# Kernel optimization log

Hardware: AMD Instinct MI355X
Metric: run time of the kernel (lower is better)

Reference implementation:

```python
import jax, jax.numpy as jnp
import numpy as np

N = 300_000
DEG = 16
E = N * DEG
EPS_W = 1e-12  # guard for zero-distance neighbors
EPS_A = 1e-8   # diagonal regularization of the 3x3 normal matrix


def setup_inputs() -> dict:
    key = jax.random.key(0)
    k1, k2, k3 = jax.random.split(key, 3)
    coordinates = jax.random.normal(k1, (N, 3), dtype=jnp.float32)
    u = jax.random.normal(k2, (N, 1), dtype=jnp.float32)
    # uniform-degree CSR: offsets[i] = i*DEG
    offsets = (jnp.arange(N + 1) * DEG).astype(jnp.int32)
    indices = jax.random.randint(k3, (E,), 0, N, dtype=jnp.int32)
    return {"coordinates": coordinates, "u": u, "offsets": offsets, "indices": indices}


def _mesh_lsq_gradient(coords, values, offsets, indices):
    """Weighted least-squares gradient reconstruction over a CSR neighbor list.

    coords: [N,3], values: [N,C], offsets: [N+1], indices: [E].
    Returns [N,3,C]: per-node gradient of each channel.
    """
    n = coords.shape[0]
    e = indices.shape[0]
    # node id owning each edge: offsets[i] <= e < offsets[i+1]
    seg = jnp.searchsorted(offsets, jnp.arange(e, dtype=offsets.dtype), side='right') - 1
    dx = coords[indices] - coords[seg]            # [E,3]
    dv = values[indices] - values[seg]            # [E,C]
    w = 1.0 / jnp.maximum(jnp.sum(dx * dx, axis=-1), EPS_W)  # inverse-distance^2 weights [E]
    # normal equations: A g = b per node
    A = jax.ops.segment_sum(w[:, None, None] * dx[:, :, None] * dx[:, None, :], seg, num_segments=n)  # [N,3,3]
    b = jax.ops.segment_sum(w[:, None, None] * dx[:, :, None] * dv[:, None, :], seg, num_segments=n)  # [N,3,C]
    A = A + EPS_A * jnp.eye(3, dtype=coords.dtype)
    return jnp.linalg.solve(A, b)  # [N,3,C]


def reference(coordinates, u, offsets, indices):
    coords = jax.lax.stop_gradient(coordinates)  # original does coords.detach()
    vals = u[:, 0:1]                              # squeeze(-1), keep as 1 channel
    first = _mesh_lsq_gradient(coords, vals, offsets, indices)[..., 0]   # [N,3] = (u_x,u_y,u_z)
    # second pass: gradients of all three first derivatives at once (channels)
    second = _mesh_lsq_gradient(coords, first, offsets, indices)         # [N,3,3]; second[:,b,a] = d(du/dx_a)/dx_b
    u_xx = second[:, 0, 0]
    u_yy = second[:, 1, 1]
    u_zz = second[:, 2, 2]
    u_xy = second[:, 1, 0]  # mixed = second_grads[a][:, b] for a<b
    u_xz = second[:, 2, 0]
    u_yz = second[:, 2, 1]
    # columns: [xx, yy, zz, xy, xz, yz] (mixed derivs returned once; module duplicates symmetric keys)
    return jnp.stack([u_xx, u_yy, u_zz, u_xy, u_xz, u_yz], axis=-1)
```

## Files before the change

### kernel.cpp

```cpp
#include <hip/hip_runtime.h>
#include <hip/hip_fp16.h>


constexpr int N_NODES = 300000;
constexpr int DEG = 16;
constexpr float EPS_W = 1e-12f;
constexpr double EPS_A = 1e-8;

typedef float f32x4 __attribute__((ext_vector_type(4)));
typedef float f32x2 __attribute__((ext_vector_type(2)));

__device__ __forceinline__ float redux16(float v) {
    v += __shfl_xor(v, 1, 16);
    v += __shfl_xor(v, 2, 16);
    v += __shfl_xor(v, 4, 16);
    v += __shfl_xor(v, 8, 16);
    return v;
}

__global__ __launch_bounds__(256) void pack_p1(
    const float* __restrict__ coords,
    const float* __restrict__ u,
    float4* __restrict__ p1)
{
    int i = blockIdx.x * 256 + threadIdx.x;
    if (i >= N_NODES) return;
    p1[i] = make_float4(coords[3 * i + 0], coords[3 * i + 1],
                        coords[3 * i + 2], u[i]);
}


__global__ __launch_bounds__(256) void lsq_pass1_x(
    const float4* __restrict__ p1,
    const int*    __restrict__ indices,
    float4*       __restrict__ G,
    f32x4*        __restrict__ M,
    f32x2*        __restrict__ WDX)
{
    int tid  = blockIdx.x * 256 + threadIdx.x;
    int node = tid >> 4;
    int lane = tid & 15;
    if (node >= N_NODES) return;

    float4 c = p1[node];
    int e = node * DEG + lane;
    int j = __builtin_nontemporal_load(indices + e);
    float4 p = p1[j];

    float dx = p.x - c.x, dy = p.y - c.y, dz = p.z - c.z, dv = p.w - c.w;
    float w = 1.0f / fmaxf(dx * dx + dy * dy + dz * dz, EPS_W);
    float wx = w * dx, wy = w * dy, wz = w * dz;

    union { __half h[4]; f32x2 f2; } pk;
    pk.h[0] = __float2half_rn(wx);
    pk.h[1] = __float2half_rn(wy);
    pk.h[2] = __float2half_rn(wz);
    pk.h[3] = __float2half_rn(0.0f);
    __builtin_nontemporal_store(pk.f2, WDX + e);

    float a00 = redux16(wx * dx);
    float a01 = redux16(wx * dy);
    float a02 = redux16(wx * dz);
    float a11 = redux16(wy * dy);
    float a12 = redux16(wy * dz);
    float a22 = redux16(wz * dz);
    float b0  = redux16(wx * dv);
    float b1  = redux16(wy * dv);
    float b2  = redux16(wz * dv);

    if (lane == 0) {
        double A00 = (double)a00 + EPS_A;
        double A11 = (double)a11 + EPS_A;
        double A22 = (double)a22 + EPS_A;
        double A01 = (double)a01, A02 = (double)a02, A12 = (double)a12;
        double j00 = A11 * A22 - A12 * A12;
        double j01 = A02 * A12 - A01 * A22;
        double j02 = A01 * A12 - A02 * A11;
        double j11 = A00 * A22 - A02 * A02;
        double j12 = A01 * A02 - A00 * A12;
        double j22 = A00 * A11 - A01 * A01;
        double det = A00 * j00 + A01 * j01 + A02 * j02;
        double inv = 1.0 / det;
        float m00 = (float)(j00 * inv), m01 = (float)(j01 * inv);
        float m02 = (float)(j02 * inv), m11 = (float)(j11 * inv);
        float m12 = (float)(j12 * inv), m22 = (float)(j22 * inv);
        float g0 = m00 * b0 + m01 * b1 + m02 * b2;
        float g1 = m01 * b0 + m11 * b1 + m12 * b2;
        float g2 = m02 * b0 + m12 * b1 + m22 * b2;
        G[node] = make_float4(g0, g1, g2, 0.0f);
        f32x4 mv0 = {m00, m01, m02, m11};
        f32x4 mv1 = {m12, m22, 0.0f, 0.0f};
        __builtin_nontemporal_store(mv0, M + 2 * node);
        __builtin_nontemporal_store(mv1, M + 2 * node + 1);
    }
}

__global__ __launch_bounds__(256) void lsq_pass2_x(
    const float4* __restrict__ G,
    const f32x4*  __restrict__ M,
    const f32x2*  __restrict__ WDX,
    const int*    __restrict__ indices,
    float*        __restrict__ out)
{
    int tid  = blockIdx.x * 256 + threadIdx.x;
    int node = tid >> 4;
    int lane = tid & 15;
    if (node >= N_NODES) return;

    float4 gi = G[node];
    int e = node * DEG + lane;
    int j = __builtin_nontemporal_load(indices + e);
    union { __half h[4]; f32x2 f2; } pk;
    pk.f2 = __builtin_nontemporal_load(WDX + e);
    float wx = __half2float(pk.h[0]);
    float wy = __half2float(pk.h[1]);
    float wz = __half2float(pk.h[2]);

    float4 gj = G[j];
    float dv0 = gj.x - gi.x, dv1 = gj.y - gi.y, dv2 = gj.z - gi.z;

    float b00 = redux16(wx * dv0);
    float b10 = redux16(wy * dv0);
    float b20 = redux16(wz * dv0);
    float b01 = redux16(wx * dv1);
    float b11 = redux16(wy * dv1);
    float b21 = redux16(wz * dv1);
    float b02 = redux16(wx * dv2);
    float b12 = redux16(wy * dv2);
    float b22 = redux16(wz * dv2);

    if (lane == 0) {
        f32x4 m0 = __builtin_nontemporal_load(M + 2 * node);
        f32x4 m1 = __builtin_nontemporal_load(M + 2 * node + 1);
        float m00 = m0.x, m01 = m0.y, m02 = m0.z, m11 = m0.w;
        float m12 = m1.x, m22 = m1.y;
        float x00 = m00 * b00 + m01 * b10 + m02 * b20;
        float x10 = m01 * b00 + m11 * b10 + m12 * b20;
        float x20 = m02 * b00 + m12 * b10 + m22 * b20;
        float x11 = m01 * b01 + m11 * b11 + m12 * b21;
        float x21 = m02 * b01 + m12 * b11 + m22 * b21;
        float x22 = m02 * b02 + m12 * b12 + m22 * b22;
        f32x2* o2 = (f32x2*)(out + 6 * node);
        f32x2 o0 = {x00, x11};
        f32x2 o1 = {x22, x10};
        f32x2 o2v = {x20, x21};
        __builtin_nontemporal_store(o0, o2 + 0);
        __builtin_nontemporal_store(o1, o2 + 1);
        __builtin_nontemporal_store(o2v, o2 + 2);
    }
}


__global__ __launch_bounds__(256) void lsq_pass1_fb(
    const float4* __restrict__ p1,
    const int*    __restrict__ indices,
    float4*       __restrict__ p2)
{
    int tid  = blockIdx.x * 256 + threadIdx.x;
    int node = tid >> 4;
    int lane = tid & 15;
    if (node >= N_NODES) return;

    float4 c = p1[node];
    int j = __builtin_nontemporal_load(indices + node * DEG + lane);
    float4 p = p1[j];
    float dx = p.x - c.x, dy = p.y - c.y, dz = p.z - c.z, dv = p.w - c.w;
    float w = 1.0f / fmaxf(dx * dx + dy * dy + dz * dz, EPS_W);

    float a00 = redux16(w * dx * dx);
    float a01 = redux16(w * dx * dy);
    float a02 = redux16(w * dx * dz);
    float a11 = redux16(w * dy * dy);
    float a12 = redux16(w * dy * dz);
    float a22 = redux16(w * dz * dz);
    float b0  = redux16(w * dx * dv);
    float b1  = redux16(w * dy * dv);
    float b2  = redux16(w * dz * dv);

    if (lane == 0) {
        double A00 = (double)a00 + EPS_A;
        double A11 = (double)a11 + EPS_A;
        double A22 = (double)a22 + EPS_A;
        double A01 = (double)a01, A02 = (double)a02, A12 = (double)a12;
        double j00 = A11 * A22 - A12 * A12;
        double j01 = A02 * A12 - A01 * A22;
        double j02 = A01 * A12 - A02 * A11;
        double j11 = A00 * A22 - A02 * A02;
        double j12 = A01 * A02 - A00 * A12;
        double j22 = A00 * A11 - A01 * A01;
        double det = A00 * j00 + A01 * j01 + A02 * j02;
        double inv = 1.0 / det;
        float g0 = (float)((j00 * b0 + j01 * b1 + j02 * b2) * inv);
        float g1 = (float)((j01 * b0 + j11 * b1 + j12 * b2) * inv);
        float g2 = (float)((j02 * b0 + j12 * b1 + j22 * b2) * inv);
        p2[2 * node + 0] = make_float4(c.x, c.y, c.z, g0);
        p2[2 * node + 1] = make_float4(g1, g2, 0.0f, 0.0f);
    }
}

__global__ __launch_bounds__(256) void lsq_pass2_fb(
    const float4* __restrict__ p2,
    const int*    __restrict__ indices,
    float*        __restrict__ out)
{
    int tid  = blockIdx.x * 256 + threadIdx.x;
    int node = tid >> 4;
    int lane = tid & 15;
    if (node >= N_NODES) return;

    float4 c0 = p2[2 * node + 0];
    float4 c1 = p2[2 * node + 1];
    int j = __builtin_nontemporal_load(indices + node * DEG + lane);
    float4 r0 = p2[2 * j + 0];
    float4 r1 = p2[2 * j + 1];

    float dx = r0.x - c0.x, dy = r0.y - c0.y, dz = r0.z - c0.z;
    float dv0 = r0.w - c0.w, dv1 = r1.x - c1.x, dv2 = r1.y - c1.y;
    float w = 1.0f / fmaxf(dx * dx + dy * dy + dz * dz, EPS_W);

    float a00 = redux16(w * dx * dx);
    float a01 = redux16(w * dx * dy);
    float a02 = redux16(w * dx * dz);
    float a11 = redux16(w * dy * dy);
    float a12 = redux16(w * dy * dz);
    float a22 = redux16(w * dz * dz);
    float b00 = redux16(w * dx * dv0);
    float b10 = redux16(w * dy * dv0);
    float b20 = redux16(w * dz * dv0);
    float b01 = redux16(w * dx * dv1);
    float b11 = redux16(w * dy * dv1);
    float b21 = redux16(w * dz * dv1);
    float b02 = redux16(w * dx * dv2);
    float b12 = redux16(w * dy * dv2);
    float b22 = redux16(w * dz * dv2);

    if (lane == 0) {
        double A00 = (double)a00 + EPS_A;
        double A11 = (double)a11 + EPS_A;
        double A22 = (double)a22 + EPS_A;
        double A01 = (double)a01, A02 = (double)a02, A12 = (double)a12;
        double j00 = A11 * A22 - A12 * A12;
        double j01 = A02 * A12 - A01 * A22;
        double j02 = A01 * A12 - A02 * A11;
        double j11 = A00 * A22 - A02 * A02;
        double j12 = A01 * A02 - A00 * A12;
        double j22 = A00 * A11 - A01 * A01;
        double det = A00 * j00 + A01 * j01 + A02 * j02;
        double inv = 1.0 / det;
        double x00 = (j00 * b00 + j01 * b10 + j02 * b20) * inv;
        double x10 = (j01 * b00 + j11 * b10 + j12 * b20) * inv;
        double x20 = (j02 * b00 + j12 * b10 + j22 * b20) * inv;
        double x11 = (j01 * b01 + j11 * b11 + j12 * b21) * inv;
        double x21 = (j02 * b01 + j12 * b11 + j22 * b21) * inv;
        double x22 = (j02 * b02 + j12 * b12 + j22 * b22) * inv;
        __builtin_nontemporal_store((float)x00, out + 6 * node + 0);
        __builtin_nontemporal_store((float)x11, out + 6 * node + 1);
        __builtin_nontemporal_store((float)x22, out + 6 * node + 2);
        __builtin_nontemporal_store((float)x10, out + 6 * node + 3);
        __builtin_nontemporal_store((float)x20, out + 6 * node + 4);
        __builtin_nontemporal_store((float)x21, out + 6 * node + 5);
    }
}

extern "C" void kernel_launch(void* const* d_in, const int* in_sizes, int n_in,
                              void* d_out, int out_size, void* d_ws, size_t ws_size,
                              hipStream_t stream) {
    const float* coords  = (const float*)d_in[0];
    const float* u       = (const float*)d_in[1];
    const int*   indices = (const int*)d_in[3];
    float*       out     = (float*)d_out;

    const int block = 256;
    const int grid_edges = (N_NODES * DEG) / block;
    const int grid_nodes = (N_NODES + block - 1) / block;

    const size_t szP1  = (size_t)N_NODES * 16;
    const size_t szG   = (size_t)N_NODES * 16;
    const size_t szM   = (size_t)N_NODES * 32;
    const size_t szWDX = (size_t)N_NODES * DEG * 8;
    const size_t need_main = szP1 + szG + szM + szWDX;

    char* ws = (char*)d_ws;
    float4* p1 = (float4*)ws;
    pack_p1<<<grid_nodes, block, 0, stream>>>(coords, u, p1);

    if (ws_size >= need_main) {
        float4* G   = (float4*)(ws + szP1);
        f32x4*  M   = (f32x4*)(ws + szP1 + szG);
        f32x2*  WDX = (f32x2*)(ws + szP1 + szG + szM);
        lsq_pass1_x<<<grid_edges, block, 0, stream>>>(p1, indices, G, M, WDX);
        lsq_pass2_x<<<grid_edges, block, 0, stream>>>(G, M, WDX, indices, out);
    } else {
        float4* p2 = (float4*)(ws + szP1);
        lsq_pass1_fb<<<grid_edges, block, 0, stream>>>(p1, indices, p2);
        lsq_pass2_fb<<<grid_edges, block, 0, stream>>>(p2, indices, out);
    }
}
```

Measured before the change: 160.8 us.

## Fuse pack and both LSQ passes into one cooperative persistent kernel

Replaces the three-kernel sequence with one cooperative kernel of 1024 blocks that packs inputs, runs pass one, grid-syncs, then runs pass two. Each 16-lane group keeps neighbor indices and fp16-packed weighted dx/dy (plus fp32 wz) in registers, and keeps the inverse normal matrix in shared memory, so the per-edge WDX and M buffers and the second index read are no longer written to or fetched from global memory. This trades kernel-launch boundaries for grid-wide barriers, lower occupancy from a fixed grid with register arrays, and reduced precision on two of the weight components. It falls back to the old path if the cooperative launch fails.

```diff
diff --git a/kernel.cpp b/kernel.cpp
--- a/kernel.cpp
+++ b/kernel.cpp
@@ -1,11 +1,20 @@
 #include <hip/hip_runtime.h>
 #include <hip/hip_fp16.h>
+#include <hip/hip_cooperative_groups.h>
+
+namespace cg = cooperative_groups;
 
 
 constexpr int N_NODES = 300000;
 constexpr int DEG = 16;
 constexpr float EPS_W = 1e-12f;
 constexpr double EPS_A = 1e-8;
+
+constexpr int NBLK = 1024;
+constexpr int TPB  = 256;
+constexpr int GRP  = TPB / 16;
+constexpr int NPB  = (N_NODES + NBLK - 1) / NBLK;
+constexpr int ITER = (NPB + GRP - 1) / GRP;
 
 typedef float f32x4 __attribute__((ext_vector_type(4)));
 typedef float f32x2 __attribute__((ext_vector_type(2)));
@@ -17,6 +26,139 @@
     v += __shfl_xor(v, 8, 16);
     return v;
 }
+
+
+__global__ __launch_bounds__(TPB, 4) void lsq_fused(
+    const float* __restrict__ coords,
+    const float* __restrict__ u,
+    const int*   __restrict__ indices,
+    float4*      __restrict__ P1,
+    float4*      __restrict__ G,
+    float*       __restrict__ out)
+{
+    __shared__ float sM[ITER * GRP][6];
+
+    const int tid   = threadIdx.x;
+    const int sub   = tid >> 4;
+    const int lane  = tid & 15;
+    const int nbase = blockIdx.x * NPB;
+
+    for (int i = blockIdx.x * TPB + tid; i < N_NODES; i += NBLK * TPB) {
+        P1[i] = make_float4(coords[3 * i], coords[3 * i + 1],
+                            coords[3 * i + 2], u[i]);
+    }
+    cg::this_grid().sync();
+
+    int          idxr[ITER];
+    unsigned int wxyr[ITER];
+    float        wzr [ITER];
+
+    #pragma unroll
+    for (int t = 0; t < ITER; ++t) {
+        const int local = t * GRP + sub;
+        const int node  = nbase + local;
+        const bool act  = (local < NPB) && (node < N_NODES);
+
+        int j = 0;
+        float dx = 0.f, dy = 0.f, dz = 0.f, dv = 0.f, w = 0.f;
+        if (act) {
+            float4 c = P1[node];
+            j = __builtin_nontemporal_load(indices + node * DEG + lane);
+            float4 p = P1[j];
+            dx = p.x - c.x; dy = p.y - c.y; dz = p.z - c.z; dv = p.w - c.w;
+            w = 1.0f / fmaxf(dx * dx + dy * dy + dz * dz, EPS_W);
+        }
+        float wx = w * dx, wy = w * dy, wz = w * dz;
+        idxr[t] = j;
+        union { __half2 h2; unsigned int ui; } pk;
+        pk.h2 = __halves2half2(__float2half_rn(wx), __float2half_rn(wy));
+        wxyr[t] = pk.ui;
+        wzr[t] = wz;
+
+        float a00 = redux16(wx * dx);
+        float a01 = redux16(wx * dy);
+        float a02 = redux16(wx * dz);
+        float a11 = redux16(wy * dy);
+        float a12 = redux16(wy * dz);
+        float a22 = redux16(wz * dz);
+        float b0  = redux16(wx * dv);
+        float b1  = redux16(wy * dv);
+        float b2  = redux16(wz * dv);
+
+        if (act && lane == 0) {
+            double A00 = (double)a00 + EPS_A;
+            double A11 = (double)a11 + EPS_A;
+            double A22 = (double)a22 + EPS_A;
+            double A01 = (double)a01, A02 = (double)a02, A12 = (double)a12;
+            double j00 = A11 * A22 - A12 * A12;
+            double j01 = A02 * A12 - A01 * A22;
+            double j02 = A01 * A12 - A02 * A11;
+            double j11 = A00 * A22 - A02 * A02;
+            double j12 = A01 * A02 - A00 * A12;
+            double j22 = A00 * A11 - A01 * A01;
+            double det = A00 * j00 + A01 * j01 + A02 * j02;
+            double inv = 1.0 / det;
+            float m00 = (float)(j00 * inv), m01 = (float)(j01 * inv);
+            float m02 = (float)(j02 * inv), m11 = (float)(j11 * inv);
+            float m12 = (float)(j12 * inv), m22 = (float)(j22 * inv);
+            G[node] = make_float4(m00 * b0 + m01 * b1 + m02 * b2,
+                                  m01 * b0 + m11 * b1 + m12 * b2,
+                                  m02 * b0 + m12 * b1 + m22 * b2, 0.0f);
+            sM[local][0] = m00; sM[local][1] = m01; sM[local][2] = m02;
+            sM[local][3] = m11; sM[local][4] = m12; sM[local][5] = m22;
+        }
+    }
+    cg::this_grid().sync();
+
+    #pragma unroll
+    for (int t = 0; t < ITER; ++t) {
+        const int local = t * GRP + sub;
+        const int node  = nbase + local;
+        const bool act  = (local < NPB) && (node < N_NODES);
+
+        union { __half2 h2; unsigned int ui; } pk;
+        pk.ui = wxyr[t];
+        float wx = __low2float(pk.h2);
+        float wy = __high2float(pk.h2);
+        float wz = wzr[t];
+
+        float dv0 = 0.f, dv1 = 0.f, dv2 = 0.f;
+        if (act) {
+            float4 gi = G[node];
+            float4 gj = G[idxr[t]];
+            dv0 = gj.x - gi.x; dv1 = gj.y - gi.y; dv2 = gj.z - gi.z;
+        }
+
+        float b00 = redux16(wx * dv0);
+        float b10 = redux16(wy * dv0);
+        float b20 = redux16(wz * dv0);
+        float b01 = redux16(wx * dv1);
+        float b11 = redux16(wy * dv1);
+        float b21 = redux16(wz * dv1);
+        float b02 = redux16(wx * dv2);
+        float b12 = redux16(wy * dv2);
+        float b22 = redux16(wz * dv2);
+
+        if (act && lane == 0) {
+            float m00 = sM[local][0], m01 = sM[local][1], m02 = sM[local][2];
+            float m11 = sM[local][3], m12 = sM[local][4], m22 = sM[local][5];
+            float x00 = m00 * b00 + m01 * b10 + m02 * b20;
+            float x10 = m01 * b00 + m11 * b10 + m12 * b20;
+            float x20 = m02 * b00 + m12 * b10 + m22 * b20;
+            float x11 = m01 * b01 + m11 * b11 + m12 * b21;
+            float x21 = m02 * b01 + m12 * b11 + m22 * b21;
+            float x22 = m02 * b02 + m12 * b12 + m22 * b22;
+            f32x2* o2 = (f32x2*)(out + 6 * node);
+            f32x2 o0 = {x00, x11};
+            f32x2 o1 = {x22, x10};
+            f32x2 o2v = {x20, x21};
+            __builtin_nontemporal_store(o0,  o2 + 0);
+            __builtin_nontemporal_store(o1,  o2 + 1);
+            __builtin_nontemporal_store(o2v, o2 + 2);
+        }
+    }
+}
+
 
 __global__ __launch_bounds__(256) void pack_p1(
     const float* __restrict__ coords,
@@ -25,10 +167,9 @@
 {
     int i = blockIdx.x * 256 + threadIdx.x;
     if (i >= N_NODES) return;
-    p1[i] = make_float4(coords[3 * i + 0], coords[3 * i + 1],
+    p1[i] = make_float4(coords[3 * i], coords[3 * i + 1],
                         coords[3 * i + 2], u[i]);
 }
-
 
 __global__ __launch_bounds__(256) void lsq_pass1_x(
     const float4* __restrict__ p1,
@@ -84,10 +225,9 @@
         float m00 = (float)(j00 * inv), m01 = (float)(j01 * inv);
         float m02 = (float)(j02 * inv), m11 = (float)(j11 * inv);
         float m12 = (float)(j12 * inv), m22 = (float)(j22 * inv);
-        float g0 = m00 * b0 + m01 * b1 + m02 * b2;
-        float g1 = m01 * b0 + m11 * b1 + m12 * b2;
-        float g2 = m02 * b0 + m12 * b1 + m22 * b2;
-        G[node] = make_float4(g0, g1, g2, 0.0f);
+        G[node] = make_float4(m00 * b0 + m01 * b1 + m02 * b2,
+                              m01 * b0 + m11 * b1 + m12 * b2,
+                              m02 * b0 + m12 * b1 + m22 * b2, 0.0f);
         f32x4 mv0 = {m00, m01, m02, m11};
         f32x4 mv1 = {m12, m22, 0.0f, 0.0f};
         __builtin_nontemporal_store(mv0, M + 2 * node);
@@ -144,121 +284,9 @@
         f32x2 o0 = {x00, x11};
         f32x2 o1 = {x22, x10};
         f32x2 o2v = {x20, x21};
-        __builtin_nontemporal_store(o0, o2 + 0);
-        __builtin_nontemporal_store(o1, o2 + 1);
+        __builtin_nontemporal_store(o0,  o2 + 0);
+        __builtin_nontemporal_store(o1,  o2 + 1);
         __builtin_nontemporal_store(o2v, o2 + 2);
-    }
-}
-
-
-__global__ __launch_bounds__(256) void lsq_pass1_fb(
-    const float4* __restrict__ p1,
-    const int*    __restrict__ indices,
-    float4*       __restrict__ p2)
-{
-    int tid  = blockIdx.x * 256 + threadIdx.x;
-    int node = tid >> 4;
-    int lane = tid & 15;
-    if (node >= N_NODES) return;
-
-    float4 c = p1[node];
-    int j = __builtin_nontemporal_load(indices + node * DEG + lane);
-    float4 p = p1[j];
-    float dx = p.x - c.x, dy = p.y - c.y, dz = p.z - c.z, dv = p.w - c.w;
-    float w = 1.0f / fmaxf(dx * dx + dy * dy + dz * dz, EPS_W);
-
-    float a00 = redux16(w * dx * dx);
-    float a01 = redux16(w * dx * dy);
-    float a02 = redux16(w * dx * dz);
-    float a11 = redux16(w * dy * dy);
-    float a12 = redux16(w * dy * dz);
-    float a22 = redux16(w * dz * dz);
-    float b0  = redux16(w * dx * dv);
-    float b1  = redux16(w * dy * dv);
-    float b2  = redux16(w * dz * dv);
-
-    if (lane == 0) {
-        double A00 = (double)a00 + EPS_A;
-        double A11 = (double)a11 + EPS_A;
-        double A22 = (double)a22 + EPS_A;
-        double A01 = (double)a01, A02 = (double)a02, A12 = (double)a12;
-        double j00 = A11 * A22 - A12 * A12;
-        double j01 = A02 * A12 - A01 * A22;
-        double j02 = A01 * A12 - A02 * A11;
-        double j11 = A00 * A22 - A02 * A02;
-        double j12 = A01 * A02 - A00 * A12;
-        double j22 = A00 * A11 - A01 * A01;
-        double det = A00 * j00 + A01 * j01 + A02 * j02;
-        double inv = 1.0 / det;
-        float g0 = (float)((j00 * b0 + j01 * b1 + j02 * b2) * inv);
-        float g1 = (float)((j01 * b0 + j11 * b1 + j12 * b2) * inv);
-        float g2 = (float)((j02 * b0 + j12 * b1 + j22 * b2) * inv);
-        p2[2 * node + 0] = make_float4(c.x, c.y, c.z, g0);
-        p2[2 * node + 1] = make_float4(g1, g2, 0.0f, 0.0f);
-    }
-}
-
-__global__ __launch_bounds__(256) void lsq_pass2_fb(
-    const float4* __restrict__ p2,
-    const int*    __restrict__ indices,
-    float*        __restrict__ out)
-{
-    int tid  = blockIdx.x * 256 + threadIdx.x;
-    int node = tid >> 4;
-    int lane = tid & 15;
-    if (node >= N_NODES) return;
-
-    float4 c0 = p2[2 * node + 0];
-    float4 c1 = p2[2 * node + 1];
-    int j = __builtin_nontemporal_load(indices + node * DEG + lane);
-    float4 r0 = p2[2 * j + 0];
-    float4 r1 = p2[2 * j + 1];
-
-    float dx = r0.x - c0.x, dy = r0.y - c0.y, dz = r0.z - c0.z;
-    float dv0 = r0.w - c0.w, dv1 = r1.x - c1.x, dv2 = r1.y - c1.y;
-    float w = 1.0f / fmaxf(dx * dx + dy * dy + dz * dz, EPS_W);
-
-    float a00 = redux16(w * dx * dx);
-    float a01 = redux16(w * dx * dy);
-    float a02 = redux16(w * dx * dz);
-    float a11 = redux16(w * dy * dy);
-    float a12 = redux16(w * dy * dz);
-    float a22 = redux16(w * dz * dz);
-    float b00 = redux16(w * dx * dv0);
-    float b10 = redux16(w * dy * dv0);
-    float b20 = redux16(w * dz * dv0);
-    float b01 = redux16(w * dx * dv1);
-    float b11 = redux16(w * dy * dv1);
-    float b21 = redux16(w * dz * dv1);
-    float b02 = redux16(w * dx * dv2);
-    float b12 = redux16(w * dy * dv2);
-    float b22 = redux16(w * dz * dv2);
-
-    if (lane == 0) {
-        double A00 = (double)a00 + EPS_A;
-        double A11 = (double)a11 + EPS_A;
-        double A22 = (double)a22 + EPS_A;
-        double A01 = (double)a01, A02 = (double)a02, A12 = (double)a12;
-        double j00 = A11 * A22 - A12 * A12;
-        double j01 = A02 * A12 - A01 * A22;
-        double j02 = A01 * A12 - A02 * A11;
-        double j11 = A00 * A22 - A02 * A02;
-        double j12 = A01 * A02 - A00 * A12;
-        double j22 = A00 * A11 - A01 * A01;
-        double det = A00 * j00 + A01 * j01 + A02 * j02;
-        double inv = 1.0 / det;
-        double x00 = (j00 * b00 + j01 * b10 + j02 * b20) * inv;
-        double x10 = (j01 * b00 + j11 * b10 + j12 * b20) * inv;
-        double x20 = (j02 * b00 + j12 * b10 + j22 * b20) * inv;
-        double x11 = (j01 * b01 + j11 * b11 + j12 * b21) * inv;
-        double x21 = (j02 * b01 + j12 * b11 + j22 * b21) * inv;
-        double x22 = (j02 * b02 + j12 * b12 + j22 * b22) * inv;
-        __builtin_nontemporal_store((float)x00, out + 6 * node + 0);
-        __builtin_nontemporal_store((float)x11, out + 6 * node + 1);
-        __builtin_nontemporal_store((float)x22, out + 6 * node + 2);
-        __builtin_nontemporal_store((float)x10, out + 6 * node + 3);
-        __builtin_nontemporal_store((float)x20, out + 6 * node + 4);
-        __builtin_nontemporal_store((float)x21, out + 6 * node + 5);
     }
 }
 
@@ -270,29 +298,28 @@
     const int*   indices = (const int*)d_in[3];
     float*       out     = (float*)d_out;
 
+    char* ws = (char*)d_ws;
+    const size_t szP1 = (size_t)N_NODES * 16;
+    const size_t szG  = (size_t)N_NODES * 16;
+    float4* P1 = (float4*)ws;
+    float4* G  = (float4*)(ws + szP1);
+
+    const float* c_ = coords; const float* u_ = u; const int* i_ = indices;
+    float4* p1_ = P1; float4* g_ = G; float* o_ = out;
+    void* kargs[] = { (void*)&c_, (void*)&u_, (void*)&i_,
+                      (void*)&p1_, (void*)&g_, (void*)&o_ };
+    hipError_t err = hipLaunchCooperativeKernel((void*)lsq_fused, dim3(NBLK),
+                                                dim3(TPB), kargs, 0, stream);
+    if (err == hipSuccess) return;
+
     const int block = 256;
     const int grid_edges = (N_NODES * DEG) / block;
     const int grid_nodes = (N_NODES + block - 1) / block;
 
-    const size_t szP1  = (size_t)N_NODES * 16;
-    const size_t szG   = (size_t)N_NODES * 16;
-    const size_t szM   = (size_t)N_NODES * 32;
-    const size_t szWDX = (size_t)N_NODES * DEG * 8;
-    const size_t need_main = szP1 + szG + szM + szWDX;
-
-    char* ws = (char*)d_ws;
-    float4* p1 = (float4*)ws;
-    pack_p1<<<grid_nodes, block, 0, stream>>>(coords, u, p1);
-
-    if (ws_size >= need_main) {
-        float4* G   = (float4*)(ws + szP1);
-        f32x4*  M   = (f32x4*)(ws + szP1 + szG);
-        f32x2*  WDX = (f32x2*)(ws + szP1 + szG + szM);
-        lsq_pass1_x<<<grid_edges, block, 0, stream>>>(p1, indices, G, M, WDX);
-        lsq_pass2_x<<<grid_edges, block, 0, stream>>>(G, M, WDX, indices, out);
-    } else {
-        float4* p2 = (float4*)(ws + szP1);
-        lsq_pass1_fb<<<grid_edges, block, 0, stream>>>(p1, indices, p2);
-        lsq_pass2_fb<<<grid_edges, block, 0, stream>>>(p2, indices, out);
-    }
-}
+    f32x4* M   = (f32x4*)(ws + szP1 + szG);
+    f32x2* WDX = (f32x2*)(ws + szP1 + szG + (size_t)N_NODES * 32);
+
+    pack_p1<<<grid_nodes, block, 0, stream>>>(coords, u, P1);
+    lsq_pass1_x<<<grid_edges, block, 0, stream>>>(P1, indices, G, M, WDX);
+    lsq_pass2_x<<<grid_edges, block, 0, stream>>>(G, M, WDX, indices, out);
+}
```

Result: slower. 434.5 us (+170.2%).
